# Kernel optimization log

Measured on AMD Instinct MI355X. Metric: run time of the kernel, lower is better.

Reference implementation:

```python
import jax, jax.numpy as jnp
import numpy as np

D = 1024
H = 16
DK = D // H
HID = 4096
EPS = 1e-5


def setup_inputs() -> dict:
    key = jax.random.key(0)
    ks = jax.random.split(key, 16)
    B, S = 2, 2048
    sc = lambda fan_in: 1.0 / np.sqrt(fan_in)
    inp = {
        "x": jax.random.normal(ks[0], (B, S, D), jnp.float32),
        "y": jax.random.normal(ks[1], (B, S, D), jnp.float32),
        "mask": jnp.ones((B, 1, 1, S), jnp.int32),
        # attention projections, stored [in, out]
        "Wq": jax.random.normal(ks[2], (D, D), jnp.float32) * sc(D),
        "bq": jnp.zeros((D,), jnp.float32),
        "Wk": jax.random.normal(ks[3], (D, D), jnp.float32) * sc(D),
        "bk": jnp.zeros((D,), jnp.float32),
        "Wv": jax.random.normal(ks[4], (D, D), jnp.float32) * sc(D),
        "bv": jnp.zeros((D,), jnp.float32),
        "Wo": jax.random.normal(ks[5], (D, D), jnp.float32) * sc(D),
        "bo": jnp.zeros((D,), jnp.float32),
        # FFN
        "W1": jax.random.normal(ks[6], (D, HID), jnp.float32) * sc(D),
        "b1": jnp.zeros((HID,), jnp.float32),
        "W2": jax.random.normal(ks[7], (HID, D), jnp.float32) * sc(HID),
        "b2": jnp.zeros((D,), jnp.float32),
        # LayerNorms
        "g1": jnp.ones((D,), jnp.float32),
        "be1": jnp.zeros((D,), jnp.float32),
        "g2": jnp.ones((D,), jnp.float32),
        "be2": jnp.zeros((D,), jnp.float32),
    }
    return inp


def _layer_norm(x, g, b):
    m = jnp.mean(x, axis=-1, keepdims=True)
    v = jnp.mean(jnp.square(x - m), axis=-1, keepdims=True)
    return (x - m) * jax.lax.rsqrt(v + EPS) * g + b


def _split_heads(t):  # [B,S,D] -> [B,H,S,DK]
    B, S, _ = t.shape
    return t.reshape(B, S, H, DK).transpose(0, 2, 1, 3)


def reference(x, y, mask, Wq, bq, Wk, bk, Wv, bv, Wo, bo,
              W1, b1, W2, b2, g1, be1, g2, be2):
    scale = 1.0 / np.sqrt(DK)
    Q = _split_heads(x @ Wq + bq)
    K = _split_heads(y @ Wk + bk)
    V = _split_heads(y @ Wv + bv)
    scores = jnp.einsum("bhqd,bhkd->bhqk", Q, K) * scale  # [B,H,S,S]
    scores = jnp.where(mask == 0, jnp.float32(-1e9), scores)
    probs = jax.nn.softmax(scores, axis=-1)
    attn = jnp.einsum("bhqk,bhkd->bhqd", probs, V)
    B, _, S, _ = attn.shape
    attn = attn.transpose(0, 2, 1, 3).reshape(B, S, D)
    mha_out = attn @ Wo + bo
    x1 = _layer_norm(x + mha_out, g1, be1)
    ff = jax.nn.relu(x1 @ W1 + b1) @ W2 + b2
    return _layer_norm(x1 + ff, g2, be2)
```

## Files before the change

### kernel.cpp

```cpp
#include <hip/hip_runtime.h>

#define S_ 2048
#define D_ 1024
#define B_ 2
#define H_ 16
#define DK_ 64
#define HID_ 4096

typedef unsigned short u16;
typedef __attribute__((ext_vector_type(8))) short short8;
typedef __attribute__((ext_vector_type(4))) short s16x4;
typedef __attribute__((ext_vector_type(4))) float f32x4;

#define SLOT(q16, r16) (((q16) * 16) + ((r16) ^ (q16)))

__device__ __forceinline__ float bf2f(u16 u) {
  return __uint_as_float(((unsigned int)u) << 16);
}
__device__ __forceinline__ u16 f2bf(float f) {
  unsigned int x = __float_as_uint(f);
  x += 0x7fff + ((x >> 16) & 1);
  return (u16)(x >> 16);
}
__device__ __forceinline__ unsigned int pk2bf(float lo, float hi) {
  return ((__float_as_uint(lo) + 0x8000u) >> 16) | ((__float_as_uint(hi) + 0x8000u) & 0xffff0000u);
}

__device__ __forceinline__ f32x4 mfma16(s16x4 a, s16x4 b, f32x4 c) {
#if __has_builtin(__builtin_amdgcn_mfma_f32_16x16x16_bf16)
  return __builtin_amdgcn_mfma_f32_16x16x16_bf16(a, b, c, 0, 0, 0);
#else
  return __builtin_amdgcn_mfma_f32_16x16x16bf16_1k(a, b, c, 0, 0, 0);
#endif
}

__global__ void prep8_k(
    const float* __restrict__ Wq, const float* __restrict__ Wk,
    const float* __restrict__ Wv, const float* __restrict__ Wo,
    const float* __restrict__ W1, const float* __restrict__ W2,
    const float* __restrict__ x, const float* __restrict__ y,
    u16* __restrict__ WqT, u16* __restrict__ WkT, u16* __restrict__ WvT,
    u16* __restrict__ WoT, u16* __restrict__ W1T, u16* __restrict__ W2T,
    u16* __restrict__ xb, u16* __restrict__ yb) {
  __shared__ u16 tile[32][33];
  const int z = blockIdx.z;
  const int tx = threadIdx.x, ty = threadIdx.y;
  if (z >= 6) {
    const float* in = (z == 7) ? y : x;
    u16* outp = (z == 7) ? yb : xb;
    const int tid = ty * 32 + tx;
    const long i = ((long)blockIdx.y * 128 + blockIdx.x) * 256 + tid;
    float4 v = ((const float4*)in)[i];
    unsigned int lo = (unsigned int)f2bf(v.x) | ((unsigned int)f2bf(v.y) << 16);
    unsigned int hi = (unsigned int)f2bf(v.z) | ((unsigned int)f2bf(v.w) << 16);
    ((uint2*)outp)[i] = make_uint2(lo, hi);
    return;
  }
  const float* in; u16* outp; int R, C;
  switch (z) {
    case 0: in = Wq; outp = WqT; R = 1024; C = 1024; break;
    case 1: in = Wk; outp = WkT; R = 1024; C = 1024; break;
    case 2: in = Wv; outp = WvT; R = 1024; C = 1024; break;
    case 3: in = Wo; outp = WoT; R = 1024; C = 1024; break;
    case 4: in = W1; outp = W1T; R = 1024; C = 4096; break;
    default: in = W2; outp = W2T; R = 4096; C = 1024; break;
  }
  int c0, r0;
  if (z == 5) { c0 = blockIdx.y * 32; r0 = blockIdx.x * 32; }
  else        { c0 = blockIdx.x * 32; r0 = blockIdx.y * 32; }
  if (c0 >= C || r0 >= R) return;
  for (int i = ty; i < 32; i += 8)
    tile[i][tx] = f2bf(in[(long)(r0 + i) * C + c0 + tx]);
  __syncthreads();
  for (int i = ty; i < 32; i += 8)
    outp[(long)(c0 + i) * R + r0 + tx] = tile[tx][i];
}

template<int MT, int NT, int OUTF32>
__global__ __launch_bounds__(256) void gemm_bt(
    const u16* __restrict__ A, const u16* __restrict__ Bt,
    const float* __restrict__ bias, void* __restrict__ Cv,
    int K, int lda, int ldb, int ldc,
    long sA, long sB, long sC, int relu) {
  constexpr int BM = MT * 32;
  constexpr int BN = NT * 32;
  __shared__ __align__(16) u16 As[BM * 32];
  __shared__ __align__(16) u16 Bs[BN * 32];
  const int z = blockIdx.z;
  A  += (long)z * sA;
  Bt += (long)z * sB;
  const int tid  = threadIdx.x;
  const int lane = tid & 63, wave = tid >> 6;
  const int quad = lane >> 4, l15 = lane & 15;
  const int wm = wave >> 1, wn = wave & 1;
  const u16* Ab = A  + (long)(blockIdx.y * BM) * lda;
  const u16* Bb = Bt + (long)(blockIdx.x * BN) * ldb;

  f32x4 acc[MT][NT];
#pragma unroll
  for (int i = 0; i < MT; ++i)
#pragma unroll
    for (int j = 0; j < NT; ++j) acc[i][j] = (f32x4){0.f, 0.f, 0.f, 0.f};

  const int r0  = tid >> 2;
  const int kk0 = (tid & 3) * 8;

  for (int kt = 0; kt < K; kt += 32) {
#pragma unroll
    for (int p = 0; p < BM / 64; ++p) {
      __builtin_amdgcn_global_load_lds(
          (const __attribute__((address_space(1))) void*)(Ab + (long)(p * 64 + r0) * lda + kt + kk0),
          (__attribute__((address_space(3))) void*)(&As[p * 2048 + tid * 8]), 16, 0, 0);
    }
#pragma unroll
    for (int p = 0; p < BN / 64; ++p) {
      __builtin_amdgcn_global_load_lds(
          (const __attribute__((address_space(1))) void*)(Bb + (long)(p * 64 + r0) * ldb + kt + kk0),
          (__attribute__((address_space(3))) void*)(&Bs[p * 2048 + tid * 8]), 16, 0, 0);
    }
    __syncthreads();
    short8 af[MT], bfr[NT];
#pragma unroll
    for (int mt = 0; mt < MT; ++mt)
      af[mt] = *(const short8*)&As[(wm * (MT * 16) + mt * 16 + l15) * 32 + quad * 8];
#pragma unroll
    for (int nt = 0; nt < NT; ++nt)
      bfr[nt] = *(const short8*)&Bs[(wn * (NT * 16) + nt * 16 + l15) * 32 + quad * 8];
#pragma unroll
    for (int mt = 0; mt < MT; ++mt)
#pragma unroll
      for (int nt = 0; nt < NT; ++nt)
        acc[mt][nt] = __builtin_amdgcn_mfma_f32_16x16x32_bf16(af[mt], bfr[nt], acc[mt][nt], 0, 0, 0);
    __syncthreads();
  }

#pragma unroll
  for (int nt = 0; nt < NT; ++nt) {
    const int col = blockIdx.x * BN + wn * (NT * 16) + nt * 16 + l15;
    const float bvv = bias ? bias[col] : 0.f;
#pragma unroll
    for (int mt = 0; mt < MT; ++mt) {
#pragma unroll
      for (int r = 0; r < 4; ++r) {
        const int row = blockIdx.y * BM + wm * (MT * 16) + mt * 16 + quad * 4 + r;
        float v = acc[mt][nt][r] + bvv;
        if (relu) v = fmaxf(v, 0.f);
        if (OUTF32) ((float*)Cv)[(long)z * sC + (long)row * ldc + col] = v;
        else        ((u16*)Cv)[(long)z * sC + (long)row * ldc + col] = f2bf(v);
      }
    }
  }
}

template<int RELU>
__global__ __launch_bounds__(512, 2) void gemm256_k(
    const u16* __restrict__ A, const u16* __restrict__ Bt,
    const float* __restrict__ bias, u16* __restrict__ C,
    int K, int lda, int ldb, int ldc, int kOff, long sC) {
  __shared__ __align__(16) u16 lds[65536];
  const int bx = blockIdx.x, by = blockIdx.y, z = blockIdx.z;
  A  += (long)z * kOff;
  Bt += (long)z * kOff;
  const int tid = threadIdx.x;
  const int lane = tid & 63, w = tid >> 6;
  const int quad = lane >> 4, l15 = lane & 15;
  const int wm = w >> 2, wn = w & 3;

  const int srow = w * 16 + l15;
  const u16* a0p = A + (long)(by * 256 + srow) * lda + quad * 8;
  const u16* a1p = a0p + (long)128 * lda;
  const u16* b0p = Bt + (long)(bx * 256 + srow) * ldb + quad * 8;
  const u16* b1p = b0p + (long)128 * ldb;

  f32x4 acc[8][4];
#pragma unroll
  for (int i = 0; i < 8; ++i)
#pragma unroll
    for (int j = 0; j < 4; ++j) acc[i][j] = (f32x4){0.f, 0.f, 0.f, 0.f};

  auto STAGE = [&](int c) {
    const int sl = (c & 3) * 8192;
    const long ko = (long)c * 32;
    __builtin_amdgcn_global_load_lds(
        (const __attribute__((address_space(1))) void*)(a0p + ko),
        (__attribute__((address_space(3))) void*)(&lds[sl + tid * 8]), 16, 0, 0);
    __builtin_amdgcn_global_load_lds(
        (const __attribute__((address_space(1))) void*)(a1p + ko),
        (__attribute__((address_space(3))) void*)(&lds[sl + 4096 + tid * 8]), 16, 0, 0);
    __builtin_amdgcn_global_load_lds(
        (const __attribute__((address_space(1))) void*)(b0p + ko),
        (__attribute__((address_space(3))) void*)(&lds[32768 + sl + tid * 8]), 16, 0, 0);
    __builtin_amdgcn_global_load_lds(
        (const __attribute__((address_space(1))) void*)(b1p + ko),
        (__attribute__((address_space(3))) void*)(&lds[32768 + sl + 4096 + tid * 8]), 16, 0, 0);
  };

  auto COMPUTE = [&](int t) {
    const int sl = (t & 3) * 8192;
    short8 af[8], bfv[4];
#pragma unroll
    for (int fr = 0; fr < 8; ++fr)
      af[fr] = *(const short8*)&lds[sl + ((wm * 8 + fr) * 64 + lane) * 8];
#pragma unroll
    for (int fc = 0; fc < 4; ++fc)
      bfv[fc] = *(const short8*)&lds[32768 + sl + ((wn * 4 + fc) * 64 + lane) * 8];
    __builtin_amdgcn_s_setprio(1);
#pragma unroll
    for (int fr = 0; fr < 8; ++fr)
#pragma unroll
      for (int fc = 0; fc < 4; ++fc)
        acc[fr][fc] = __builtin_amdgcn_mfma_f32_16x16x32_bf16(af[fr], bfv[fc], acc[fr][fc], 0, 0, 0);
    __builtin_amdgcn_s_setprio(0);
  };

  const int NT = K >> 5;
  STAGE(0); STAGE(1); STAGE(2);
  for (int t = 0; t < NT - 2; ++t) {
    asm volatile("s_waitcnt vmcnt(8)" ::: "memory");
    __builtin_amdgcn_s_barrier();
    __builtin_amdgcn_sched_barrier(0);
    if (t + 3 < NT) STAGE(t + 3);
    COMPUTE(t);
  }
  asm volatile("s_waitcnt vmcnt(4)" ::: "memory");
  __builtin_amdgcn_s_barrier();
  __builtin_amdgcn_sched_barrier(0);
  COMPUTE(NT - 2);
  asm volatile("s_waitcnt vmcnt(0)" ::: "memory");
  __builtin_amdgcn_s_barrier();
  __builtin_amdgcn_sched_barrier(0);
  COMPUTE(NT - 1);

  C += (long)z * sC;
#pragma unroll
  for (int fc = 0; fc < 4; ++fc) {
    const int col = bx * 256 + wn * 64 + fc * 16 + l15;
    const float bvv = bias ? bias[col] : 0.f;
#pragma unroll
    for (int fr = 0; fr < 8; ++fr) {
      const long row = by * 256 + wm * 128 + fr * 16 + quad * 4;
#pragma unroll
      for (int r = 0; r < 4; ++r) {
        float v = acc[fr][fc][r] + bvv;
        if (RELU) v = fmaxf(v, 0.f);
        C[(row + r) * ldc + col] = f2bf(v);
      }
    }
  }
}

__global__ __launch_bounds__(256) void qkv_k(
    const u16* __restrict__ xb, const u16* __restrict__ yb,
    const u16* __restrict__ WqT, const u16* __restrict__ WkT, const u16* __restrict__ WvT,
    const float* __restrict__ bq, const float* __restrict__ bk, const float* __restrict__ bv,
    u16* __restrict__ Q, u16* __restrict__ Kp, u16* __restrict__ Vp) {
  __shared__ __align__(16) u16 As[128 * 32];
  __shared__ __align__(16) u16 Bs[128 * 32];
  const int z = blockIdx.z;
  const u16* A  = (z == 0) ? xb : yb;
  const u16* Bt = (z == 0) ? WqT : (z == 1) ? WkT : WvT;
  const float* bias = (z == 0) ? bq : (z == 1) ? bk : bv;
  u16* C = (z == 0) ? Q : (z == 1) ? Kp : Vp;
  const float sc = (z == 0) ? 0.18033688011112042f : 1.0f;
  const int tid  = threadIdx.x;
  const int lane = tid & 63, wave = tid >> 6;
  const int quad = lane >> 4, l15 = lane & 15;
  const int wm = wave >> 1, wn = wave & 1;
  const u16* Ab = A  + (long)(blockIdx.y * 128) * D_;
  const u16* Bb = Bt + (long)(blockIdx.x * 128) * D_;

  f32x4 acc[4][4];
#pragma unroll
  for (int i = 0; i < 4; ++i)
#pragma unroll
    for (int j = 0; j < 4; ++j) acc[i][j] = (f32x4){0.f, 0.f, 0.f, 0.f};

  const int r0  = tid >> 2;
  const int kk0 = (tid & 3) * 8;

  for (int kt = 0; kt < D_; kt += 32) {
#pragma unroll
    for (int p = 0; p < 2; ++p) {
      __builtin_amdgcn_global_load_lds(
          (const __attribute__((address_space(1))) void*)(Ab + (long)(p * 64 + r0) * D_ + kt + kk0),
          (__attribute__((address_space(3))) void*)(&As[p * 2048 + tid * 8]), 16, 0, 0);
      __builtin_amdgcn_global_load_lds(
          (const __attribute__((address_space(1))) void*)(Bb + (long)(p * 64 + r0) * D_ + kt + kk0),
          (__attribute__((address_space(3))) void*)(&Bs[p * 2048 + tid * 8]), 16, 0, 0);
    }
    __syncthreads();
    short8 af[4], bfr[4];
#pragma unroll
    for (int mt = 0; mt < 4; ++mt)
      af[mt] = *(const short8*)&As[(wm * 64 + mt * 16 + l15) * 32 + quad * 8];
#pragma unroll
    for (int nt = 0; nt < 4; ++nt)
      bfr[nt] = *(const short8*)&Bs[(wn * 64 + nt * 16 + l15) * 32 + quad * 8];
#pragma unroll
    for (int mt = 0; mt < 4; ++mt)
#pragma unroll
      for (int nt = 0; nt < 4; ++nt)
        acc[mt][nt] = __builtin_amdgcn_mfma_f32_16x16x32_bf16(af[mt], bfr[nt], acc[mt][nt], 0, 0, 0);
    __syncthreads();
  }

#pragma unroll
  for (int nt = 0; nt < 4; ++nt) {
    const int col = blockIdx.x * 128 + wn * 64 + nt * 16 + l15;
    const float bvv = bias[col];
#pragma unroll
    for (int mt = 0; mt < 4; ++mt) {
#pragma unroll
      for (int r = 0; r < 4; ++r) {
        const int row = blockIdx.y * 128 + wm * 64 + mt * 16 + quad * 4 + r;
        C[(long)row * D_ + col] = f2bf((acc[mt][nt][r] + bvv) * sc);
      }
    }
  }
}

__global__ void vtrans_k(const u16* __restrict__ V, u16* __restrict__ Vt) {
  __shared__ u16 tile[32][33];
  const int bh = blockIdx.z, b = bh >> 4, h = bh & 15;
  const u16* in = V + (long)b * S_ * D_ + h * DK_;
  u16* outp = Vt + (long)bh * DK_ * S_;
  const int s0 = blockIdx.x * 32, d0 = blockIdx.y * 32;
  const int tx = threadIdx.x, ty = threadIdx.y;
  for (int i = ty; i < 32; i += 8)
    tile[i][tx] = in[(long)(s0 + i) * D_ + d0 + tx];
  __syncthreads();
  for (int i = ty; i < 32; i += 8)
    outp[(long)(d0 + i) * S_ + s0 + tx] = tile[tx][i];
}

__global__ __launch_bounds__(512, 2) void flash_k(
    const u16* __restrict__ Q, const u16* __restrict__ Kp, const u16* __restrict__ Vt,
    const int* __restrict__ mask, u16* __restrict__ ctx) {
  __shared__ __align__(16) u16 sQ[16384];
  __shared__ __align__(16) u16 sK[2][2048];
  __shared__ __align__(16) u16 sV[2][2048];
  __shared__ int s_allones;

  const int bh = blockIdx.x, qt = blockIdx.y;
  const int b = bh >> 4, h = bh & 15;
  const int tid = threadIdx.x;
  const int w = tid >> 6, lane = tid & 63;
  const int quad = lane >> 4, l15 = lane & 15;

  const u16* Qg  = Q  + ((long)b * S_ + qt * 256) * D_ + h * DK_;
  const u16* Kg  = Kp + (long)b * S_ * D_ + h * DK_;
  const u16* Vtg = Vt + (long)bh * DK_ * S_;
  const int* maskg = mask + (long)b * S_;
  u16* ctxg = ctx + ((long)b * S_ + qt * 256) * D_ + h * DK_;

  const int isK = tid < 256;
  const int t2 = tid & 255;
  const int krow = t2 >> 3, kc = t2 & 7;
  const int vd  = ((t2 >> 6) << 4) | (t2 & 15);
  const int vq4 = ((t2 >> 4) & 3) * 4;
  const u16* gptr = isK ? (Kg + (long)krow * D_ + kc * 8)
                        : (Vtg + (long)vd * S_ + vq4);
  const long gstep = isK ? (long)32 * D_ : (long)32;
  const int ksw = (((krow >> 4) * 2 + (kc >> 2)) * 64 + SLOT(kc & 3, krow & 15)) * 8;
  u16* sdst0 = isK ? &sK[0][ksw] : &sV[0][t2 * 8];
  u16* sdst1 = isK ? &sK[1][ksw] : &sV[1][t2 * 8];

  auto gload = [&](const u16* p) {
    uint4 r;
    if (isK) {
      r = *(const uint4*)p;
    } else {
      uint2 lo = *(const uint2*)p;
      uint2 hi = *(const uint2*)(p + 16);
      r = make_uint4(lo.x, lo.y, hi.x, hi.y);
    }
    return r;
  };

  uint4 reg = gload(gptr);

  int part = 1;
  for (int i = tid; i < S_; i += 512) part &= (maskg[i] != 0);
  if (tid == 0) s_allones = 1;

#pragma unroll
  for (int p = 0; p < 4; ++p) {
    const int idx = p * 512 + tid;
    const int row = idx >> 3, cb = idx & 7;
    uint4 v = *(const uint4*)(Qg + (long)row * D_ + cb * 8);
    *(uint4*)&sQ[(((row >> 4) * 2 + (cb >> 2)) * 64 + SLOT(cb & 3, row & 15)) * 8] = v;
  }
  *(uint4*)sdst0 = reg;
  reg = gload(gptr + gstep);
  gptr += 2 * gstep;
  __syncthreads();

  const int rslot = SLOT(quad, l15) * 8;

  short8 qf[2][2];
#pragma unroll
  for (int mf = 0; mf < 2; ++mf)
#pragma unroll
    for (int kt = 0; kt < 2; ++kt)
      qf[mf][kt] = *(const short8*)&sQ[(((w * 2 + mf) * 2 + kt) * 64) * 8 + rslot];

  if (!part) s_allones = 0;
  __syncthreads();
  const int allones = s_allones;

  float lsum[2] = {0.f, 0.f};
  f32x4 accOT[2][4];
#pragma unroll
  for (int i = 0; i < 2; ++i)
#pragma unroll
    for (int j = 0; j < 4; ++j) accOT[i][j] = (f32x4){0.f, 0.f, 0.f, 0.f};

  for (int t = 0; t < 64; ++t) {
    if (t) __syncthreads();
    const int buf = t & 1;
    if (t < 63) {
      *(uint4*)((t & 1) ? sdst0 : sdst1) = reg;
      if (t < 62) {
        reg = gload(gptr);
        gptr += gstep;
      }
    }
    f32x4 accS[2][2];
#pragma unroll
    for (int i = 0; i < 2; ++i)
#pragma unroll
      for (int j = 0; j < 2; ++j) accS[i][j] = (f32x4){0.f, 0.f, 0.f, 0.f};
#pragma unroll
    for (int kt = 0; kt < 2; ++kt) {
      short8 kf0 = *(const short8*)&sK[buf][(kt * 64) * 8 + rslot];
      short8 kf1 = *(const short8*)&sK[buf][((2 + kt) * 64) * 8 + rslot];
#pragma unroll
      for (int mf = 0; mf < 2; ++mf) {
        accS[0][mf] = __builtin_amdgcn_mfma_f32_16x16x32_bf16(kf0, qf[mf][kt], accS[0][mf], 0, 0, 0);
        accS[1][mf] = __builtin_amdgcn_mfma_f32_16x16x32_bf16(kf1, qf[mf][kt], accS[1][mf], 0, 0, 0);
      }
    }
    s16x4 pb[2][2];
    if (allones) {
#pragma unroll
      for (int mk = 0; mk < 2; ++mk)
#pragma unroll
        for (int mf = 0; mf < 2; ++mf) {
          float p0 = __builtin_amdgcn_exp2f(accS[mk][mf][0]);
          float p1 = __builtin_amdgcn_exp2f(accS[mk][mf][1]);
          float p2 = __builtin_amdgcn_exp2f(accS[mk][mf][2]);
          float p3 = __builtin_amdgcn_exp2f(accS[mk][mf][3]);
          lsum[mf] += (p0 + p1) + (p2 + p3);
          *(uint2*)&pb[mk][mf] = make_uint2(pk2bf(p0, p1), pk2bf(p2, p3));
        }
    } else {
      const int4 mv0 = *(const int4*)(maskg + t * 32 + quad * 4);
      const int4 mv1 = *(const int4*)(maskg + t * 32 + 16 + quad * 4);
#pragma unroll
      for (int mk = 0; mk < 2; ++mk) {
        const int4 mv = mk ? mv1 : mv0;
#pragma unroll
        for (int mf = 0; mf < 2; ++mf) {
          float p0 = mv.x ? __builtin_amdgcn_exp2f(accS[mk][mf][0]) : 0.f;
          float p1 = mv.y ? __builtin_amdgcn_exp2f(accS[mk][mf][1]) : 0.f;
          float p2 = mv.z ? __builtin_amdgcn_exp2f(accS[mk][mf][2]) : 0.f;
          float p3 = mv.w ? __builtin_amdgcn_exp2f(accS[mk][mf][3]) : 0.f;
          lsum[mf] += (p0 + p1) + (p2 + p3);
          *(uint2*)&pb[mk][mf] = make_uint2(pk2bf(p0, p1), pk2bf(p2, p3));
        }
      }
    }
#pragma unroll
    for (int n = 0; n < 4; ++n) {
      short8 vv = *(const short8*)&sV[buf][(n * 64 + lane) * 8];
      s16x4 v0 = __builtin_shufflevector(vv, vv, 0, 1, 2, 3);
      s16x4 v1 = __builtin_shufflevector(vv, vv, 4, 5, 6, 7);
#pragma unroll
      for (int mf = 0; mf < 2; ++mf) {
        accOT[mf][n] = mfma16(v0, pb[0][mf], accOT[mf][n]);
        accOT[mf][n] = mfma16(v1, pb[1][mf], accOT[mf][n]);
      }
    }
  }

#pragma unroll
  for (int mf = 0; mf < 2; ++mf) {
    lsum[mf] += __shfl_xor(lsum[mf], 16, 64);
    lsum[mf] += __shfl_xor(lsum[mf], 32, 64);
  }
  const float inv0 = 1.f / lsum[0], inv1 = 1.f / lsum[1];
#pragma unroll
  for (int mf = 0; mf < 2; ++mf) {
    const float iv = mf ? inv1 : inv0;
    u16* cp = ctxg + (long)(w * 32 + mf * 16 + l15) * D_;
#pragma unroll
    for (int n = 0; n < 4; ++n) {
      float o0 = accOT[mf][n][0] * iv;
      float o1 = accOT[mf][n][1] * iv;
      float o2 = accOT[mf][n][2] * iv;
      float o3 = accOT[mf][n][3] * iv;
      *(uint2*)(cp + n * 16 + quad * 4) = make_uint2(pk2bf(o0, o1), pk2bf(o2, o3));
    }
  }
}

__device__ __forceinline__ float block_reduce_sum(float v, float* red) {
#pragma unroll
  for (int off = 32; off; off >>= 1) v += __shfl_down(v, off, 64);
  __syncthreads();
  if ((threadIdx.x & 63) == 0) red[threadIdx.x >> 6] = v;
  __syncthreads();
  return red[0] + red[1] + red[2] + red[3];
}

__global__ __launch_bounds__(256) void addln_fb(const float* __restrict__ A,
    const u16* __restrict__ M0, const u16* __restrict__ M1, const float* __restrict__ bo,
    const float* __restrict__ g, const float* __restrict__ be, u16* __restrict__ outp) {
  __shared__ float red[4];
  const int row = blockIdx.x, tid = threadIdx.x;
  const float4 av = ((const float4*)(A + (long)row * D_))[tid];
  const uint2 m0 = ((const uint2*)(M0 + (long)row * D_))[tid];
  const uint2 m1 = ((const uint2*)(M1 + (long)row * D_))[tid];
  const int c0 = tid * 4;
  float xv[4];
  xv[0] = av.x + bf2f((u16)(m0.x & 0xffff)) + bf2f((u16)(m1.x & 0xffff)) + bo[c0 + 0];
  xv[1] = av.y + bf2f((u16)(m0.x >> 16))    + bf2f((u16)(m1.x >> 16))    + bo[c0 + 1];
  xv[2] = av.z + bf2f((u16)(m0.y & 0xffff)) + bf2f((u16)(m1.y & 0xffff)) + bo[c0 + 2];
  xv[3] = av.w + bf2f((u16)(m0.y >> 16))    + bf2f((u16)(m1.y >> 16))    + bo[c0 + 3];
  float s  = xv[0] + xv[1] + xv[2] + xv[3];
  float ss = xv[0]*xv[0] + xv[1]*xv[1] + xv[2]*xv[2] + xv[3]*xv[3];
  s  = block_reduce_sum(s, red);
  ss = block_reduce_sum(ss, red);
  const float m   = s * (1.0f / 1024.0f);
  const float var = ss * (1.0f / 1024.0f) - m * m;
  const float rs  = rsqrtf(var + 1e-5f);
  float v0 = (xv[0] - m) * rs * g[c0 + 0] + be[c0 + 0];
  float v1 = (xv[1] - m) * rs * g[c0 + 1] + be[c0 + 1];
  float v2 = (xv[2] - m) * rs * g[c0 + 2] + be[c0 + 2];
  float v3 = (xv[3] - m) * rs * g[c0 + 3] + be[c0 + 3];
  unsigned int o01 = (unsigned int)f2bf(v0) | ((unsigned int)f2bf(v1) << 16);
  unsigned int o23 = (unsigned int)f2bf(v2) | ((unsigned int)f2bf(v3) << 16);
  ((uint2*)(outp + (long)row * D_))[tid] = make_uint2(o01, o23);
}

__global__ __launch_bounds__(256) void addln2_bf(const u16* __restrict__ A,
    const u16* __restrict__ F0, const u16* __restrict__ F1,
    const u16* __restrict__ F2, const u16* __restrict__ F3,
    const float* __restrict__ b2,
    const float* __restrict__ g, const float* __restrict__ be, float* __restrict__ outp) {
  __shared__ float red[4];
  const int row = blockIdx.x, tid = threadIdx.x;
  const uint2 av = ((const uint2*)(A + (long)row * D_))[tid];
  const uint2 f0 = ((const uint2*)(F0 + (long)row * D_))[tid];
  const uint2 f1 = ((const uint2*)(F1 + (long)row * D_))[tid];
  const uint2 f2 = ((const uint2*)(F2 + (long)row * D_))[tid];
  const uint2 f3 = ((const uint2*)(F3 + (long)row * D_))[tid];
  const int c0 = tid * 4;
  float xv[4];
  xv[0] = bf2f((u16)(av.x & 0xffff)) + bf2f((u16)(f0.x & 0xffff)) + bf2f((u16)(f1.x & 0xffff))
        + bf2f((u16)(f2.x & 0xffff)) + bf2f((u16)(f3.x & 0xffff)) + b2[c0 + 0];
  xv[1] = bf2f((u16)(av.x >> 16))    + bf2f((u16)(f0.x >> 16))    + bf2f((u16)(f1.x >> 16))
        + bf2f((u16)(f2.x >> 16))    + bf2f((u16)(f3.x >> 16))    + b2[c0 + 1];
  xv[2] = bf2f((u16)(av.y & 0xffff)) + bf2f((u16)(f0.y & 0xffff)) + bf2f((u16)(f1.y & 0xffff))
        + bf2f((u16)(f2.y & 0xffff)) + bf2f((u16)(f3.y & 0xffff)) + b2[c0 + 2];
  xv[3] = bf2f((u16)(av.y >> 16))    + bf2f((u16)(f0.y >> 16))    + bf2f((u16)(f1.y >> 16))
        + bf2f((u16)(f2.y >> 16))    + bf2f((u16)(f3.y >> 16))    + b2[c0 + 3];
  float s  = xv[0] + xv[1] + xv[2] + xv[3];
  float ss = xv[0]*xv[0] + xv[1]*xv[1] + xv[2]*xv[2] + xv[3]*xv[3];
  s  = block_reduce_sum(s, red);
  ss = block_reduce_sum(ss, red);
  const float m   = s * (1.0f / 1024.0f);
  const float var = ss * (1.0f / 1024.0f) - m * m;
  const float rs  = rsqrtf(var + 1e-5f);
  float4 o;
  o.x = (xv[0] - m) * rs * g[c0 + 0] + be[c0 + 0];
  o.y = (xv[1] - m) * rs * g[c0 + 1] + be[c0 + 1];
  o.z = (xv[2] - m) * rs * g[c0 + 2] + be[c0 + 2];
  o.w = (xv[3] - m) * rs * g[c0 + 3] + be[c0 + 3];
  ((float4*)(outp + (long)row * D_))[tid] = o;
}

extern "C" void kernel_launch(void* const* d_in, const int* in_sizes, int n_in,
                              void* d_out, int out_size, void* d_ws, size_t ws_size,
                              hipStream_t stream) {
  const float* x   = (const float*)d_in[0];
  const float* y   = (const float*)d_in[1];
  const int* mask  = (const int*)d_in[2];
  const float* Wq = (const float*)d_in[3];  const float* bq = (const float*)d_in[4];
  const float* Wk = (const float*)d_in[5];  const float* bk = (const float*)d_in[6];
  const float* Wv = (const float*)d_in[7];  const float* bv = (const float*)d_in[8];
  const float* Wo = (const float*)d_in[9];  const float* bo = (const float*)d_in[10];
  const float* W1 = (const float*)d_in[11]; const float* b1 = (const float*)d_in[12];
  const float* W2 = (const float*)d_in[13]; const float* b2 = (const float*)d_in[14];
  const float* g1 = (const float*)d_in[15]; const float* be1 = (const float*)d_in[16];
  const float* g2 = (const float*)d_in[17]; const float* be2 = (const float*)d_in[18];
  float* out = (float*)d_out;

  char* w = (char*)d_ws;
  const size_t MB = 1024 * 1024;
  u16* WqT = (u16*)(w + 0 * MB);
  u16* WkT = (u16*)(w + 2 * MB);
  u16* WvT = (u16*)(w + 4 * MB);
  u16* WoT = (u16*)(w + 6 * MB);
  u16* W1T = (u16*)(w + 8 * MB);
  u16* W2T = (u16*)(w + 16 * MB);
  u16* xb  = (u16*)(w + 24 * MB);
  u16* yb  = (u16*)(w + 32 * MB);
  u16* Q   = (u16*)(w + 40 * MB);
  u16* Kp  = (u16*)(w + 48 * MB);
  u16* Vp  = (u16*)(w + 56 * MB);
  u16* Vt  = (u16*)(w + 64 * MB);
  u16* ctx = (u16*)(w + 72 * MB);
  u16* mha = (u16*)(w + 80 * MB);
  u16* x1  = (u16*)(w + 24 * MB);
  u16* h1  = (u16*)(w + 96 * MB);
  u16* ff  = (u16*)(w + 40 * MB);

  prep8_k<<<dim3(128, 32, 8), dim3(32, 8), 0, stream>>>(Wq, Wk, Wv, Wo, W1, W2,
      x, y, WqT, WkT, WvT, WoT, W1T, W2T, xb, yb);

  qkv_k<<<dim3(8, 32, 3), 256, 0, stream>>>(xb, yb, WqT, WkT, WvT, bq, bk, bv, Q, Kp, Vp);

  vtrans_k<<<dim3(64, 2, 32), dim3(32, 8), 0, stream>>>(Vp, Vt);

  flash_k<<<dim3(32, 8), 512, 0, stream>>>(Q, Kp, Vt, mask, ctx);

  gemm_bt<4, 4, 0><<<dim3(8, 32, 2), 256, 0, stream>>>(ctx, WoT, nullptr, mha,
      512, 1024, 1024, 1024, 512, 512, (long)4096 * 1024, 0);
  addln_fb<<<dim3(4096), 256, 0, stream>>>(x, mha, mha + (long)4096 * 1024, bo, g1, be1, x1);

  gemm256_k<1><<<dim3(16, 16, 1), 512, 0, stream>>>(x1, W1T, b1, h1,
      1024, 1024, 1024, 4096, 0, 0);
  gemm256_k<0><<<dim3(4, 16, 4), 512, 0, stream>>>(h1, W2T, nullptr, ff,
      1024, 4096, 4096, 1024, 1024, (long)4096 * 1024);
  addln2_bf<<<dim3(4096), 256, 0, stream>>>(x1, ff, ff + (long)4096 * 1024,
      ff + (long)2 * 4096 * 1024, ff + (long)3 * 4096 * 1024, b2, g2, be2, out);
}
```

Measured before the change: 390.2 us.

## Fuse V transpose into QKV epilogue and software-pipeline QK^T in flash

The QKV projection kernel now writes V directly in head-transposed layout through a shared-memory staging tile, which removes the separate vtrans kernel launch and its extra global round trip. The flash attention loop is also software-pipelined: the scores for the next K tile are computed with MFMA ahead of time, while the current tile's exp and PV MFMAs run. This costs extra shared memory in qkv_k, more registers in flash_k, and an added barrier per iteration.

```diff
diff --git a/kernel.cpp b/kernel.cpp
--- a/kernel.cpp
+++ b/kernel.cpp
@@ -253,14 +253,14 @@
     const u16* __restrict__ xb, const u16* __restrict__ yb,
     const u16* __restrict__ WqT, const u16* __restrict__ WkT, const u16* __restrict__ WvT,
     const float* __restrict__ bq, const float* __restrict__ bk, const float* __restrict__ bv,
-    u16* __restrict__ Q, u16* __restrict__ Kp, u16* __restrict__ Vp) {
+    u16* __restrict__ Q, u16* __restrict__ Kp, u16* __restrict__ Vt) {
   __shared__ __align__(16) u16 As[128 * 32];
   __shared__ __align__(16) u16 Bs[128 * 32];
+  __shared__ __align__(16) u16 vt[64 * 136];
   const int z = blockIdx.z;
   const u16* A  = (z == 0) ? xb : yb;
   const u16* Bt = (z == 0) ? WqT : (z == 1) ? WkT : WvT;
   const float* bias = (z == 0) ? bq : (z == 1) ? bk : bv;
-  u16* C = (z == 0) ? Q : (z == 1) ? Kp : Vp;
   const float sc = (z == 0) ? 0.18033688011112042f : 1.0f;
   const int tid  = threadIdx.x;
   const int lane = tid & 63, wave = tid >> 6;
@@ -304,33 +304,49 @@
     __syncthreads();
   }
 
-#pragma unroll
-  for (int nt = 0; nt < 4; ++nt) {
-    const int col = blockIdx.x * 128 + wn * 64 + nt * 16 + l15;
-    const float bvv = bias[col];
-#pragma unroll
-    for (int mt = 0; mt < 4; ++mt) {
-#pragma unroll
-      for (int r = 0; r < 4; ++r) {
-        const int row = blockIdx.y * 128 + wm * 64 + mt * 16 + quad * 4 + r;
-        C[(long)row * D_ + col] = f2bf((acc[mt][nt][r] + bvv) * sc);
-      }
-    }
-  }
-}
-
-__global__ void vtrans_k(const u16* __restrict__ V, u16* __restrict__ Vt) {
-  __shared__ u16 tile[32][33];
-  const int bh = blockIdx.z, b = bh >> 4, h = bh & 15;
-  const u16* in = V + (long)b * S_ * D_ + h * DK_;
-  u16* outp = Vt + (long)bh * DK_ * S_;
-  const int s0 = blockIdx.x * 32, d0 = blockIdx.y * 32;
-  const int tx = threadIdx.x, ty = threadIdx.y;
-  for (int i = ty; i < 32; i += 8)
-    tile[i][tx] = in[(long)(s0 + i) * D_ + d0 + tx];
-  __syncthreads();
-  for (int i = ty; i < 32; i += 8)
-    outp[(long)(d0 + i) * S_ + s0 + tx] = tile[tx][i];
+  if (z != 2) {
+    u16* C = (z == 0) ? Q : Kp;
+#pragma unroll
+    for (int nt = 0; nt < 4; ++nt) {
+      const int col = blockIdx.x * 128 + wn * 64 + nt * 16 + l15;
+      const float bvv = bias[col];
+#pragma unroll
+      for (int mt = 0; mt < 4; ++mt) {
+#pragma unroll
+        for (int r = 0; r < 4; ++r) {
+          const int row = blockIdx.y * 128 + wm * 64 + mt * 16 + quad * 4 + r;
+          C[(long)row * D_ + col] = f2bf((acc[mt][nt][r] + bvv) * sc);
+        }
+      }
+    }
+  } else {
+    const int brow = blockIdx.y * 128;
+    const int b = brow >> 11;
+#pragma unroll
+    for (int hh = 0; hh < 2; ++hh) {
+      if (wn == hh) {
+#pragma unroll
+        for (int nt = 0; nt < 4; ++nt) {
+          const int dl = nt * 16 + l15;
+          const float bvv = bias[blockIdx.x * 128 + hh * 64 + dl];
+#pragma unroll
+          for (int mt = 0; mt < 4; ++mt) {
+#pragma unroll
+            for (int r = 0; r < 4; ++r)
+              vt[dl * 136 + wm * 64 + mt * 16 + quad * 4 + r] = f2bf(acc[mt][nt][r] + bvv);
+          }
+        }
+      }
+      __syncthreads();
+      const int d = tid >> 2, sl = (tid & 3) * 32;
+      const int h = blockIdx.x * 2 + hh;
+      u16* dst = Vt + ((long)(b * 16 + h) * DK_ + d) * S_ + (brow & 2047) + sl;
+#pragma unroll
+      for (int c = 0; c < 4; ++c)
+        *(uint4*)(dst + c * 8) = *(const uint4*)&vt[d * 136 + sl + c * 8];
+      if (hh == 0) __syncthreads();
+    }
+  }
 }
 
 __global__ __launch_bounds__(512, 2) void flash_k(
@@ -404,6 +420,22 @@
     for (int kt = 0; kt < 2; ++kt)
       qf[mf][kt] = *(const short8*)&sQ[(((w * 2 + mf) * 2 + kt) * 64) * 8 + rslot];
 
+  f32x4 sc_[2][2], sn_[2][2];
+#pragma unroll
+  for (int i = 0; i < 2; ++i)
+#pragma unroll
+    for (int j = 0; j < 2; ++j) sc_[i][j] = (f32x4){0.f, 0.f, 0.f, 0.f};
+#pragma unroll
+  for (int kt = 0; kt < 2; ++kt) {
+    short8 kf0 = *(const short8*)&sK[0][(kt * 64) * 8 + rslot];
+    short8 kf1 = *(const short8*)&sK[0][((2 + kt) * 64) * 8 + rslot];
+#pragma unroll
+    for (int mf = 0; mf < 2; ++mf) {
+      sc_[0][mf] = __builtin_amdgcn_mfma_f32_16x16x32_bf16(kf0, qf[mf][kt], sc_[0][mf], 0, 0, 0);
+      sc_[1][mf] = __builtin_amdgcn_mfma_f32_16x16x32_bf16(kf1, qf[mf][kt], sc_[1][mf], 0, 0, 0);
+    }
+  }
+
   if (!part) s_allones = 0;
   __syncthreads();
   const int allones = s_allones;
@@ -424,20 +456,21 @@
         reg = gload(gptr);
         gptr += gstep;
       }
-    }
-    f32x4 accS[2][2];
-#pragma unroll
-    for (int i = 0; i < 2; ++i)
-#pragma unroll
-      for (int j = 0; j < 2; ++j) accS[i][j] = (f32x4){0.f, 0.f, 0.f, 0.f};
-#pragma unroll
-    for (int kt = 0; kt < 2; ++kt) {
-      short8 kf0 = *(const short8*)&sK[buf][(kt * 64) * 8 + rslot];
-      short8 kf1 = *(const short8*)&sK[buf][((2 + kt) * 64) * 8 + rslot];
-#pragma unroll
-      for (int mf = 0; mf < 2; ++mf) {
-        accS[0][mf] = __builtin_amdgcn_mfma_f32_16x16x32_bf16(kf0, qf[mf][kt], accS[0][mf], 0, 0, 0);
-        accS[1][mf] = __builtin_amdgcn_mfma_f32_16x16x32_bf16(kf1, qf[mf][kt], accS[1][mf], 0, 0, 0);
+      __syncthreads();
+      const int nb = buf ^ 1;
+#pragma unroll
+      for (int i = 0; i < 2; ++i)
+#pragma unroll
+        for (int j = 0; j < 2; ++j) sn_[i][j] = (f32x4){0.f, 0.f, 0.f, 0.f};
+#pragma unroll
+      for (int kt = 0; kt < 2; ++kt) {
+        short8 kf0 = *(const short8*)&sK[nb][(kt * 64) * 8 + rslot];
+        short8 kf1 = *(const short8*)&sK[nb][((2 + kt) * 64) * 8 + rslot];
+#pragma unroll
+        for (int mf = 0; mf < 2; ++mf) {
+          sn_[0][mf] = __builtin_amdgcn_mfma_f32_16x16x32_bf16(kf0, qf[mf][kt], sn_[0][mf], 0, 0, 0);
+          sn_[1][mf] = __builtin_amdgcn_mfma_f32_16x16x32_bf16(kf1, qf[mf][kt], sn_[1][mf], 0, 0, 0);
+        }
       }
     }
     s16x4 pb[2][2];
@@ -446,10 +479,10 @@
       for (int mk = 0; mk < 2; ++mk)
 #pragma unroll
         for (int mf = 0; mf < 2; ++mf) {
-          float p0 = __builtin_amdgcn_exp2f(accS[mk][mf][0]);
-          float p1 = __builtin_amdgcn_exp2f(accS[mk][mf][1]);
-          float p2 = __builtin_amdgcn_exp2f(accS[mk][mf][2]);
-          float p3 = __builtin_amdgcn_exp2f(accS[mk][mf][3]);
+          float p0 = __builtin_amdgcn_exp2f(sc_[mk][mf][0]);
+          float p1 = __builtin_amdgcn_exp2f(sc_[mk][mf][1]);
+          float p2 = __builtin_amdgcn_exp2f(sc_[mk][mf][2]);
+          float p3 = __builtin_amdgcn_exp2f(sc_[mk][mf][3]);
           lsum[mf] += (p0 + p1) + (p2 + p3);
           *(uint2*)&pb[mk][mf] = make_uint2(pk2bf(p0, p1), pk2bf(p2, p3));
         }
@@ -461,10 +494,10 @@
         const int4 mv = mk ? mv1 : mv0;
 #pragma unroll
         for (int mf = 0; mf < 2; ++mf) {
-          float p0 = mv.x ? __builtin_amdgcn_exp2f(accS[mk][mf][0]) : 0.f;
-          float p1 = mv.y ? __builtin_amdgcn_exp2f(accS[mk][mf][1]) : 0.f;
-          float p2 = mv.z ? __builtin_amdgcn_exp2f(accS[mk][mf][2]) : 0.f;
-          float p3 = mv.w ? __builtin_amdgcn_exp2f(accS[mk][mf][3]) : 0.f;
+          float p0 = mv.x ? __builtin_amdgcn_exp2f(sc_[mk][mf][0]) : 0.f;
+          float p1 = mv.y ? __builtin_amdgcn_exp2f(sc_[mk][mf][1]) : 0.f;
+          float p2 = mv.z ? __builtin_amdgcn_exp2f(sc_[mk][mf][2]) : 0.f;
+          float p3 = mv.w ? __builtin_amdgcn_exp2f(sc_[mk][mf][3]) : 0.f;
           lsum[mf] += (p0 + p1) + (p2 + p3);
           *(uint2*)&pb[mk][mf] = make_uint2(pk2bf(p0, p1), pk2bf(p2, p3));
         }
@@ -481,6 +514,10 @@
         accOT[mf][n] = mfma16(v1, pb[1][mf], accOT[mf][n]);
       }
     }
+#pragma unroll
+    for (int i = 0; i < 2; ++i)
+#pragma unroll
+      for (int j = 0; j < 2; ++j) sc_[i][j] = sn_[i][j];
   }
 
 #pragma unroll
@@ -608,7 +645,6 @@
   u16* yb  = (u16*)(w + 32 * MB);
   u16* Q   = (u16*)(w + 40 * MB);
   u16* Kp  = (u16*)(w + 48 * MB);
-  u16* Vp  = (u16*)(w + 56 * MB);
   u16* Vt  = (u16*)(w + 64 * MB);
   u16* ctx = (u16*)(w + 72 * MB);
   u16* mha = (u16*)(w + 80 * MB);
@@ -619,9 +655,7 @@
   prep8_k<<<dim3(128, 32, 8), dim3(32, 8), 0, stream>>>(Wq, Wk, Wv, Wo, W1, W2,
       x, y, WqT, WkT, WvT, WoT, W1T, W2T, xb, yb);
 
-  qkv_k<<<dim3(8, 32, 3), 256, 0, stream>>>(xb, yb, WqT, WkT, WvT, bq, bk, bv, Q, Kp, Vp);
-
-  vtrans_k<<<dim3(64, 2, 32), dim3(32, 8), 0, stream>>>(Vp, Vt);
+  qkv_k<<<dim3(8, 32, 3), 256, 0, stream>>>(xb, yb, WqT, WkT, WvT, bq, bk, bv, Q, Kp, Vt);
 
   flash_k<<<dim3(32, 8), 512, 0, stream>>>(Q, Kp, Vt, mask, ctx);
 
```

New measurement: 406.0 us. 1.04x slower.
